# Kernel tuning notes

Measured on AMD Instinct MI355X. Metric: run time of the kernel, lower is better.

## Reference

```python
import jax, jax.numpy as jnp
import numpy as np


def setup_inputs() -> dict:
    key = jax.random.key(0)
    x = jax.random.normal(key, (8, 128, 64, 64), dtype=jnp.float32)
    return {"x": x}


def reference(x) -> jnp.ndarray:
    # x: [B, d, c, c]; original uses a raw view (row-major reshape), not a permute.
    B, d, c, _ = x.shape
    n = c * c
    fch = x.reshape(B, n, d)                      # [B, N, d] reinterpretation of memory
    # self-similarity attention (no scaling): softmax(fch @ fch^T)
    attn = jax.nn.softmax(jnp.einsum('bnd,bmd->bnm', fch, fch), axis=-1)  # [B, N, N]
    out = jnp.einsum('bnd,bnm->bdm', fch, attn)   # fch^T @ attn -> [B, d, N]
    return out.reshape(B, d, c, c)
```

## Files before the change

kernel.cpp:

```cpp
#include <hip/hip_runtime.h>


typedef __attribute__((ext_vector_type(8))) __bf16 bf16x8;
typedef __attribute__((ext_vector_type(4))) float f32x4;
typedef __attribute__((ext_vector_type(4))) unsigned int u32x4;

#define MFMA16(a, b, c) __builtin_amdgcn_mfma_f32_16x16x32_bf16((a), (b), (c), 0, 0, 0)
#define GLOAD16(g, l)                                                       \
  __builtin_amdgcn_global_load_lds(                                         \
      (const __attribute__((address_space(1))) void*)(g),                   \
      (__attribute__((address_space(3))) void*)(l), 16, 0, 0)
#define GLOAD4(g, l)                                                        \
  __builtin_amdgcn_global_load_lds(                                         \
      (const __attribute__((address_space(1))) void*)(g),                   \
      (__attribute__((address_space(3))) void*)(l), 4, 0, 0)

static constexpr int NT = 4096;
static constexpr int DD = 128;
static constexpr float L2E = 1.4426950408889634f;

__device__ __forceinline__ unsigned short bfc(float f) {
  return __builtin_bit_cast(unsigned short, (__bf16)f);
}
__device__ __forceinline__ float bf2f(unsigned short u) {
  return (float)__builtin_bit_cast(__bf16, u);
}

__global__ __launch_bounds__(256) void cab_prep(const float* __restrict__ x,
                                                ushort* __restrict__ Fbb,
                                                ushort* __restrict__ Ftb,
                                                float* __restrict__ nrm,
                                                float* __restrict__ bmax) {
  const int blk = blockIdx.x;
  const int b = blk & 7, n0 = (blk >> 3) * 64;
  const float* F = x + ((size_t)b * NT + n0) * DD;
  ushort* Fo = Fbb + ((size_t)b * NT + n0) * DD;
  ushort* To = Ftb + (size_t)b * DD * NT + n0;

  __shared__ ushort T[128 * 66];
  __shared__ float redw[4];

  const int t = threadIdx.x, seg = t & 15, rl = t >> 4;
  float lmax = 0.f;

#pragma unroll
  for (int i = 0; i < 4; ++i) {
    const int r = i * 16 + rl;
    float4 u = *(const float4*)(F + (size_t)r * DD + seg * 8);
    float4 v = *(const float4*)(F + (size_t)r * DD + seg * 8 + 4);
    ushort w[8] = {bfc(u.x), bfc(u.y), bfc(u.z), bfc(u.w),
                   bfc(v.x), bfc(v.y), bfc(v.z), bfc(v.w)};
    *(ushort4*)(Fo + (size_t)r * DD + seg * 8) = make_ushort4(w[0], w[1], w[2], w[3]);
    *(ushort4*)(Fo + (size_t)r * DD + seg * 8 + 4) = make_ushort4(w[4], w[5], w[6], w[7]);
    float s = 0.f;
#pragma unroll
    for (int j = 0; j < 8; ++j) {
      T[(seg * 8 + j) * 66 + r] = w[j];
      float f = bf2f(w[j]);
      s = fmaf(f, f, s);
    }
#pragma unroll
    for (int off = 1; off < 16; off <<= 1) s += __shfl_xor(s, off, 64);
    float rn = sqrtf(s);
    if (seg == 0) nrm[(size_t)b * NT + n0 + r] = rn;
    lmax = fmaxf(lmax, rn);
  }
#pragma unroll
  for (int off = 1; off < 64; off <<= 1) lmax = fmaxf(lmax, __shfl_xor(lmax, off, 64));
  if ((t & 63) == 0) redw[t >> 6] = lmax;
  __syncthreads();
  if (t == 0) bmax[blk] = fmaxf(fmaxf(redw[0], redw[1]), fmaxf(redw[2], redw[3]));

#pragma unroll
  for (int i = 0; i < 4; ++i) {
    int idx = i * 256 + t;
    int d = idx >> 3, ch = idx & 7;
    const ushort* p = &T[d * 66 + ch * 8];
    u32x4 q;
    q[0] = *(const unsigned*)(p + 0);
    q[1] = *(const unsigned*)(p + 2);
    q[2] = *(const unsigned*)(p + 4);
    q[3] = *(const unsigned*)(p + 6);
    *(u32x4*)(To + (size_t)d * NT + ch * 8) = q;
  }
}

__global__ __launch_bounds__(64) void cab_mx(const float* __restrict__ bmax,
                                             float* __restrict__ mxf) {
  const int b = blockIdx.x, l = threadIdx.x;
  float m = bmax[l * 8 + b];
#pragma unroll
  for (int off = 1; off < 64; off <<= 1) m = fmaxf(m, __shfl_xor(m, off, 64));
  if (l == 0) mxf[b] = m;
}

__global__ __launch_bounds__(256, 4) void cab_rowstats(const ushort* __restrict__ Fbb,
                                                       const float* __restrict__ nrm,
                                                       const float* __restrict__ mxf,
                                                       float* __restrict__ c2g) {
  const int b = blockIdx.x & 7;
  const int nb = (blockIdx.x >> 3) * 64;
  const ushort* Fb = Fbb + (size_t)b * NT * DD;

  const int t = threadIdx.x, lane = t & 63, wv = t >> 6;
  const int lcol = lane & 15, hi = lane >> 4;
  const int nh = wv >> 1, mq = wv & 1;

  __shared__ __align__(16) char FmB[2][16384];
  __shared__ float zred[64];

  int fmoff[4];
#pragma unroll
  for (int i = 0; i < 4; ++i) {
    int L = i * 256 + t;
    int m = L >> 4, c = (L & 15) ^ (m & 15);
    fmoff[i] = m * DD + c * 8;
  }

  bf16x8 afr[2][4];
#pragma unroll
  for (int nt = 0; nt < 2; ++nt)
#pragma unroll
    for (int ks = 0; ks < 4; ++ks)
      afr[nt][ks] = *(const bf16x8*)(Fb + (size_t)(nb + nh * 32 + nt * 16 + lcol) * DD +
                                     ks * 32 + hi * 8);

  const float mxv = mxf[b] * L2E;
  float nsh[8];
#pragma unroll
  for (int nt = 0; nt < 2; ++nt)
#pragma unroll
    for (int r = 0; r < 4; ++r)
      nsh[nt * 4 + r] = -nrm[(size_t)b * NT + nb + nh * 32 + nt * 16 + hi * 4 + r] * mxv;

#pragma unroll
  for (int i = 0; i < 4; ++i) GLOAD16(Fb + fmoff[i], &FmB[0][i * 4096 + wv * 1024]);
  __syncthreads();

  float zloc[8];
#pragma unroll
  for (int i = 0; i < 8; ++i) zloc[i] = 0.f;

  for (int s = 0; s < 64; ++s) {
    const int cur = s & 1;
    if (s < 63) {
      const ushort* src = Fb + (size_t)(s + 1) * 64 * DD;
#pragma unroll
      for (int i = 0; i < 4; ++i)
        GLOAD16(src + fmoff[i], &FmB[cur ^ 1][i * 4096 + wv * 1024]);
    }

    f32x4 sacc[2][2];
#pragma unroll
    for (int nt = 0; nt < 2; ++nt)
#pragma unroll
      for (int ms = 0; ms < 2; ++ms) sacc[nt][ms] = (f32x4){0.f, 0.f, 0.f, 0.f};
#pragma unroll
    for (int ms = 0; ms < 2; ++ms)
#pragma unroll
      for (int ks = 0; ks < 4; ++ks) {
        int ml = mq * 32 + ms * 16 + lcol;
        bf16x8 bb = *(const bf16x8*)&FmB[cur][ml * 256 + (((ks * 4 + hi) ^ lcol) << 4)];
#pragma unroll
        for (int nt = 0; nt < 2; ++nt) sacc[nt][ms] = MFMA16(afr[nt][ks], bb, sacc[nt][ms]);
      }
#pragma unroll
    for (int nt = 0; nt < 2; ++nt)
#pragma unroll
      for (int r = 0; r < 4; ++r)
        zloc[nt * 4 + r] += __builtin_amdgcn_exp2f(fmaf(sacc[nt][0][r], L2E, nsh[nt * 4 + r])) +
                            __builtin_amdgcn_exp2f(fmaf(sacc[nt][1][r], L2E, nsh[nt * 4 + r]));
    __syncthreads();
  }

#pragma unroll
  for (int i = 0; i < 8; ++i) {
#pragma unroll
    for (int off = 1; off < 16; off <<= 1) zloc[i] += __shfl_xor(zloc[i], off, 64);
  }
  if (mq == 1 && lcol == 0) {
#pragma unroll
    for (int i = 0; i < 8; ++i) zred[nh * 32 + (i >> 2) * 16 + hi * 4 + (i & 3)] = zloc[i];
  }
  __syncthreads();
  if (mq == 0 && lcol == 0) {
#pragma unroll
    for (int i = 0; i < 8; ++i) {
      int nloc = nh * 32 + (i >> 2) * 16 + hi * 4 + (i & 3);
      c2g[(size_t)b * NT + nb + nloc] = nsh[i] - __log2f(zloc[i] + zred[nloc]);
    }
  }
}

__global__ __launch_bounds__(256, 2) void cab_out(const ushort* __restrict__ Fbb,
                                                  const ushort* __restrict__ Ftb,
                                                  const float* __restrict__ c2g,
                                                  float* __restrict__ out) {
  const int b = blockIdx.x & 7, mb0 = (blockIdx.x >> 3) * 64;
  const ushort* Fb = Fbb + (size_t)b * NT * DD;
  const ushort* Ft = Ftb + (size_t)b * DD * NT;
  const float* c2p = c2g + (size_t)b * NT;

  const int t = threadIdx.x, lane = t & 63, wv = t >> 6;
  const int lcol = lane & 15, hi = lane >> 4;
  const int mh = wv & 1, nh = wv >> 1;

  __shared__ __align__(16) char LB[42496];
  char* FnB = LB;
  char* FttB = LB + 16384;
  char* Wt = LB + 32768;
  float* c2l = (float*)(LB + 41984);

  int fnoff[4], fttoff[4];
#pragma unroll
  for (int i = 0; i < 4; ++i) {
    int L = i * 256 + t;
    int n = L >> 4, cn = (L & 15) ^ (n & 15);
    fnoff[i] = n * DD + cn * 8;
    int d = L >> 3, cd = (L & 7) ^ (d & 7);
    fttoff[i] = d * NT + cd * 8;
  }

  bf16x8 fmf[2][4];
#pragma unroll
  for (int ms = 0; ms < 2; ++ms)
#pragma unroll
    for (int ks = 0; ks < 4; ++ks)
      fmf[ms][ks] = *(const bf16x8*)(Fb + (size_t)(mb0 + mh * 32 + ms * 16 + lcol) * DD +
                                     ks * 32 + hi * 8);

  f32x4 accO[8][2];
#pragma unroll
  for (int dt = 0; dt < 8; ++dt)
#pragma unroll
    for (int ms = 0; ms < 2; ++ms) accO[dt][ms] = (f32x4){0.f, 0.f, 0.f, 0.f};

#pragma unroll
  for (int i = 0; i < 4; ++i) GLOAD16(Fb + fnoff[i], &FnB[i * 4096 + wv * 1024]);
#pragma unroll
  for (int i = 0; i < 4; ++i) GLOAD16(Ft + fttoff[i], &FttB[i * 4096 + wv * 1024]);
  if (wv == 0) GLOAD4(c2p + lane, &c2l[0]);
  __syncthreads();

  const unsigned wtbase = wv * 2304;

  for (int s = 0; s < 64; ++s) {
    f32x4 sacc[2][2];
#pragma unroll
    for (int nt = 0; nt < 2; ++nt)
#pragma unroll
      for (int ms = 0; ms < 2; ++ms) sacc[nt][ms] = (f32x4){0.f, 0.f, 0.f, 0.f};
#pragma unroll
    for (int nt = 0; nt < 2; ++nt)
#pragma unroll
      for (int ks = 0; ks < 4; ++ks) {
        int n = (nh * 2 + nt) * 16 + lcol;
        bf16x8 a = *(const bf16x8*)&FnB[n * 256 + (((ks * 4 + hi) ^ lcol) << 4)];
#pragma unroll
        for (int ms = 0; ms < 2; ++ms) sacc[nt][ms] = MFMA16(a, fmf[ms][ks], sacc[nt][ms]);
      }
    bf16x8 a2[8];
#pragma unroll
    for (int dt = 0; dt < 8; ++dt)
      a2[dt] = *(const bf16x8*)&FttB[(dt * 16 + lcol) * 128 +
                                     (((nh * 4 + hi) ^ (lcol & 7)) << 4)];

    __syncthreads();

    if (s < 63) {
      const ushort* fs = Fb + (size_t)(s + 1) * 64 * DD;
      const ushort* ts = Ft + (s + 1) * 64;
#pragma unroll
      for (int i = 0; i < 4; ++i) GLOAD16(fs + fnoff[i], &FnB[i * 4096 + wv * 1024]);
#pragma unroll
      for (int i = 0; i < 4; ++i) GLOAD16(ts + fttoff[i], &FttB[i * 4096 + wv * 1024]);
      if (wv == 0) GLOAD4(c2p + (s + 1) * 64 + lane, &c2l[((s + 1) & 1) * 64]);
    }

#pragma unroll
    for (int nt = 0; nt < 2; ++nt) {
      float4 cv = *(const float4*)&c2l[(s & 1) * 64 + nh * 32 + nt * 16 + hi * 4];
#pragma unroll
      for (int ms = 0; ms < 2; ++ms) {
        ushort4 wp;
        wp.x = bfc(__builtin_amdgcn_exp2f(fmaf(sacc[nt][ms][0], L2E, cv.x)));
        wp.y = bfc(__builtin_amdgcn_exp2f(fmaf(sacc[nt][ms][1], L2E, cv.y)));
        wp.z = bfc(__builtin_amdgcn_exp2f(fmaf(sacc[nt][ms][2], L2E, cv.z)));
        wp.w = bfc(__builtin_amdgcn_exp2f(fmaf(sacc[nt][ms][3], L2E, cv.w)));
        *(ushort4*)&Wt[wtbase + (ms * 16 + lcol) * 72 + nt * 32 + hi * 8] = wp;
      }
    }
    bf16x8 b2[2];
#pragma unroll
    for (int ms = 0; ms < 2; ++ms) {
      const char* p = &Wt[wtbase + (ms * 16 + lcol) * 72 + hi * 16];
      uint2 lo = *(const uint2*)p;
      uint2 h2 = *(const uint2*)(p + 8);
      b2[ms] = __builtin_bit_cast(bf16x8, (u32x4){lo.x, lo.y, h2.x, h2.y});
    }
#pragma unroll
    for (int dt = 0; dt < 8; ++dt)
#pragma unroll
      for (int ms = 0; ms < 2; ++ms) accO[dt][ms] = MFMA16(a2[dt], b2[ms], accO[dt][ms]);

    __syncthreads();
  }

  float* red = (float*)LB;
  if (nh == 1) {
#pragma unroll
    for (int dt = 0; dt < 8; ++dt)
#pragma unroll
      for (int ms = 0; ms < 2; ++ms)
#pragma unroll
        for (int r = 0; r < 4; ++r)
          red[mh * 4096 + (dt * 8 + ms * 4 + r) * 64 + lane] = accO[dt][ms][r];
  }
  __syncthreads();
  if (nh == 0) {
    float* Ob = out + (size_t)b * DD * NT;
#pragma unroll
    for (int dt = 0; dt < 8; ++dt)
#pragma unroll
      for (int ms = 0; ms < 2; ++ms)
#pragma unroll
        for (int r = 0; r < 4; ++r) {
          float v = accO[dt][ms][r] + red[mh * 4096 + (dt * 8 + ms * 4 + r) * 64 + lane];
          Ob[(size_t)(dt * 16 + hi * 4 + r) * NT + mb0 + mh * 32 + ms * 16 + lcol] = v;
        }
  }
}

extern "C" void kernel_launch(void* const* d_in, const int* in_sizes, int n_in,
                              void* d_out, int out_size, void* d_ws, size_t ws_size,
                              hipStream_t stream) {
  const float* x = (const float*)d_in[0];
  float* out = (float*)d_out;
  char* ws = (char*)d_ws;
  ushort* Fbb = (ushort*)ws;
  ushort* Ftb = (ushort*)(ws + (8u << 20));
  float* nrm = (float*)(ws + (16u << 20));
  float* bmax = (float*)(ws + (16u << 20) + 131072);
  float* mxf = (float*)(ws + (16u << 20) + 133120);
  float* c2 = (float*)(ws + (16u << 20) + 134144);

  hipLaunchKernelGGL(cab_prep, dim3(512), dim3(256), 0, stream, x, Fbb, Ftb, nrm, bmax);
  hipLaunchKernelGGL(cab_mx, dim3(8), dim3(64), 0, stream, bmax, mxf);
  hipLaunchKernelGGL(cab_rowstats, dim3(512), dim3(256), 0, stream, Fbb, nrm, mxf, c2);
  hipLaunchKernelGGL(cab_out, dim3(512), dim3(256), 0, stream, Fbb, Ftb, c2, out);
}
```

Measured before the change: 139.7 us.

## Split key dimension in half across blocks for rowstats and output kernels

Doubles the grid of both the row-statistics and output kernels by splitting the 4096-long key loop into two halves. Partial softmax denominators are written to a scratch buffer and combined by a new small kernel that computes the log-normaliser. Output partials are accumulated with float atomicAdd into a zeroed output. This targets low occupancy: 512 blocks on a 256-CU part, with cab_out limited to two blocks per CU. The cost is an extra memset, an extra launch, and atomic traffic on the output.

```diff
diff --git a/kernel.cpp b/kernel.cpp
--- a/kernel.cpp
+++ b/kernel.cpp
@@ -97,9 +97,10 @@
 __global__ __launch_bounds__(256, 4) void cab_rowstats(const ushort* __restrict__ Fbb,
                                                        const float* __restrict__ nrm,
                                                        const float* __restrict__ mxf,
-                                                       float* __restrict__ c2g) {
+                                                       float* __restrict__ zpart) {
   const int b = blockIdx.x & 7;
-  const int nb = (blockIdx.x >> 3) * 64;
+  const int nb = ((blockIdx.x >> 3) & 63) * 64;
+  const int mhalf = blockIdx.x >> 9;
   const ushort* Fb = Fbb + (size_t)b * NT * DD;
 
   const int t = threadIdx.x, lane = t & 63, wv = t >> 6;
@@ -133,18 +134,19 @@
     for (int r = 0; r < 4; ++r)
       nsh[nt * 4 + r] = -nrm[(size_t)b * NT + nb + nh * 32 + nt * 16 + hi * 4 + r] * mxv;
 
-#pragma unroll
-  for (int i = 0; i < 4; ++i) GLOAD16(Fb + fmoff[i], &FmB[0][i * 4096 + wv * 1024]);
+  const ushort* Fm0 = Fb + (size_t)mhalf * 2048 * DD;
+#pragma unroll
+  for (int i = 0; i < 4; ++i) GLOAD16(Fm0 + fmoff[i], &FmB[0][i * 4096 + wv * 1024]);
   __syncthreads();
 
   float zloc[8];
 #pragma unroll
   for (int i = 0; i < 8; ++i) zloc[i] = 0.f;
 
-  for (int s = 0; s < 64; ++s) {
+  for (int s = 0; s < 32; ++s) {
     const int cur = s & 1;
-    if (s < 63) {
-      const ushort* src = Fb + (size_t)(s + 1) * 64 * DD;
+    if (s < 31) {
+      const ushort* src = Fm0 + (size_t)(s + 1) * 64 * DD;
 #pragma unroll
       for (int i = 0; i < 4; ++i)
         GLOAD16(src + fmoff[i], &FmB[cur ^ 1][i * 4096 + wv * 1024]);
@@ -187,16 +189,28 @@
 #pragma unroll
     for (int i = 0; i < 8; ++i) {
       int nloc = nh * 32 + (i >> 2) * 16 + hi * 4 + (i & 3);
-      c2g[(size_t)b * NT + nb + nloc] = nsh[i] - __log2f(zloc[i] + zred[nloc]);
-    }
-  }
+      zpart[(size_t)mhalf * 8 * NT + (size_t)b * NT + nb + nloc] = zloc[i] + zred[nloc];
+    }
+  }
+}
+
+__global__ __launch_bounds__(256) void cab_c2(const float* __restrict__ zpart,
+                                              const float* __restrict__ nrm,
+                                              const float* __restrict__ mxf,
+                                              float* __restrict__ c2g) {
+  int i = blockIdx.x * 256 + threadIdx.x;
+  int b = i >> 12;
+  float z = zpart[i] + zpart[8 * NT + i];
+  float nsh = -nrm[i] * (mxf[b] * L2E);
+  c2g[i] = nsh - __log2f(z);
 }
 
 __global__ __launch_bounds__(256, 2) void cab_out(const ushort* __restrict__ Fbb,
                                                   const ushort* __restrict__ Ftb,
                                                   const float* __restrict__ c2g,
                                                   float* __restrict__ out) {
-  const int b = blockIdx.x & 7, mb0 = (blockIdx.x >> 3) * 64;
+  const int b = blockIdx.x & 7, mb0 = ((blockIdx.x >> 3) & 63) * 64;
+  const int s0 = (blockIdx.x >> 9) * 32, s1 = s0 + 32;
   const ushort* Fb = Fbb + (size_t)b * NT * DD;
   const ushort* Ft = Ftb + (size_t)b * DD * NT;
   const float* c2p = c2g + (size_t)b * NT;
@@ -236,15 +250,17 @@
     for (int ms = 0; ms < 2; ++ms) accO[dt][ms] = (f32x4){0.f, 0.f, 0.f, 0.f};
 
 #pragma unroll
-  for (int i = 0; i < 4; ++i) GLOAD16(Fb + fnoff[i], &FnB[i * 4096 + wv * 1024]);
-#pragma unroll
-  for (int i = 0; i < 4; ++i) GLOAD16(Ft + fttoff[i], &FttB[i * 4096 + wv * 1024]);
-  if (wv == 0) GLOAD4(c2p + lane, &c2l[0]);
+  for (int i = 0; i < 4; ++i)
+    GLOAD16(Fb + (size_t)s0 * 64 * DD + fnoff[i], &FnB[i * 4096 + wv * 1024]);
+#pragma unroll
+  for (int i = 0; i < 4; ++i)
+    GLOAD16(Ft + s0 * 64 + fttoff[i], &FttB[i * 4096 + wv * 1024]);
+  if (wv == 0) GLOAD4(c2p + s0 * 64 + lane, &c2l[(s0 & 1) * 64]);
   __syncthreads();
 
   const unsigned wtbase = wv * 2304;
 
-  for (int s = 0; s < 64; ++s) {
+  for (int s = s0; s < s1; ++s) {
     f32x4 sacc[2][2];
 #pragma unroll
     for (int nt = 0; nt < 2; ++nt)
@@ -267,7 +283,7 @@
 
     __syncthreads();
 
-    if (s < 63) {
+    if (s < s1 - 1) {
       const ushort* fs = Fb + (size_t)(s + 1) * 64 * DD;
       const ushort* ts = Ft + (s + 1) * 64;
 #pragma unroll
@@ -326,7 +342,7 @@
 #pragma unroll
         for (int r = 0; r < 4; ++r) {
           float v = accO[dt][ms][r] + red[mh * 4096 + (dt * 8 + ms * 4 + r) * 64 + lane];
-          Ob[(size_t)(dt * 16 + hi * 4 + r) * NT + mb0 + mh * 32 + ms * 16 + lcol] = v;
+          atomicAdd(&Ob[(size_t)(dt * 16 + hi * 4 + r) * NT + mb0 + mh * 32 + ms * 16 + lcol], v);
         }
   }
 }
@@ -343,9 +359,13 @@
   float* bmax = (float*)(ws + (16u << 20) + 131072);
   float* mxf = (float*)(ws + (16u << 20) + 133120);
   float* c2 = (float*)(ws + (16u << 20) + 134144);
+  float* zpart = (float*)(ws + (16u << 20) + 265216);
+
+  hipMemsetAsync(out, 0, (size_t)out_size * sizeof(float), stream);
 
   hipLaunchKernelGGL(cab_prep, dim3(512), dim3(256), 0, stream, x, Fbb, Ftb, nrm, bmax);
   hipLaunchKernelGGL(cab_mx, dim3(8), dim3(64), 0, stream, bmax, mxf);
-  hipLaunchKernelGGL(cab_rowstats, dim3(512), dim3(256), 0, stream, Fbb, nrm, mxf, c2);
-  hipLaunchKernelGGL(cab_out, dim3(512), dim3(256), 0, stream, Fbb, Ftb, c2, out);
-}
+  hipLaunchKernelGGL(cab_rowstats, dim3(1024), dim3(256), 0, stream, Fbb, nrm, mxf, zpart);
+  hipLaunchKernelGGL(cab_c2, dim3(128), dim3(256), 0, stream, zpart, nrm, mxf, c2);
+  hipLaunchKernelGGL(cab_out, dim3(1024), dim3(256), 0, stream, Fbb, Ftb, c2, out);
+}
```

Result: slower. 171.1 us (+22.4%).

## Pre-swizzle transposed features into MFMA fragment layout and double-buffer Fn tile

Applied to the files above, without the earlier changes.

The prep kernel now writes the transposed bf16 features in a layout that matches the MFMA A-fragment order of the output kernel. The output kernel can then load each lane's a2 operands straight from global memory into registers, with no staging through LDS. The freed LDS holds a second Fn buffer, so the next tile is prefetched into the other buffer at the start of each iteration and the middle __syncthreads is dropped. The trade-off is more per-iteration global/L2 traffic going directly to registers, whose latency must be hidden by the score MFMAs and the softmax step.

```diff
diff --git a/kernel.cpp b/kernel.cpp
--- a/kernel.cpp
+++ b/kernel.cpp
@@ -28,16 +28,16 @@
 
 __global__ __launch_bounds__(256) void cab_prep(const float* __restrict__ x,
                                                 ushort* __restrict__ Fbb,
-                                                ushort* __restrict__ Ftb,
+                                                ushort* __restrict__ FtF,
                                                 float* __restrict__ nrm,
                                                 float* __restrict__ bmax) {
   const int blk = blockIdx.x;
   const int b = blk & 7, n0 = (blk >> 3) * 64;
   const float* F = x + ((size_t)b * NT + n0) * DD;
   ushort* Fo = Fbb + ((size_t)b * NT + n0) * DD;
-  ushort* To = Ftb + (size_t)b * DD * NT + n0;
-
-  __shared__ ushort T[128 * 66];
+  ushort* To = FtF + (size_t)b * DD * NT;
+
+  __shared__ ushort T[128 * 68];
   __shared__ float redw[4];
 
   const int t = threadIdx.x, seg = t & 15, rl = t >> 4;
@@ -55,7 +55,7 @@
     float s = 0.f;
 #pragma unroll
     for (int j = 0; j < 8; ++j) {
-      T[(seg * 8 + j) * 66 + r] = w[j];
+      T[(seg * 8 + j) * 68 + r] = w[j];
       float f = bf2f(w[j]);
       s = fmaf(f, f, s);
     }
@@ -74,14 +74,13 @@
 #pragma unroll
   for (int i = 0; i < 4; ++i) {
     int idx = i * 256 + t;
-    int d = idx >> 3, ch = idx & 7;
-    const ushort* p = &T[d * 66 + ch * 8];
-    u32x4 q;
-    q[0] = *(const unsigned*)(p + 0);
-    q[1] = *(const unsigned*)(p + 2);
-    q[2] = *(const unsigned*)(p + 4);
-    q[3] = *(const unsigned*)(p + 6);
-    *(u32x4*)(To + (size_t)d * NT + ch * 8) = q;
+    int nh = idx >> 9, dt = (idx >> 6) & 7, ln = idx & 63;
+    int d = dt * 16 + (ln & 15), nl = nh * 32 + (ln >> 4) * 8;
+    const ushort* p = &T[d * 68 + nl];
+    uint2 q0 = *(const uint2*)p;
+    uint2 q1 = *(const uint2*)(p + 4);
+    u32x4 q = {q0.x, q0.y, q1.x, q1.y};
+    *(u32x4*)(To + (size_t)(((n0 >> 6) * 2 + nh) * 8 + dt) * 512 + ln * 8) = q;
   }
 }
 
@@ -193,12 +192,12 @@
 }
 
 __global__ __launch_bounds__(256, 2) void cab_out(const ushort* __restrict__ Fbb,
-                                                  const ushort* __restrict__ Ftb,
+                                                  const ushort* __restrict__ FtF,
                                                   const float* __restrict__ c2g,
                                                   float* __restrict__ out) {
   const int b = blockIdx.x & 7, mb0 = (blockIdx.x >> 3) * 64;
   const ushort* Fb = Fbb + (size_t)b * NT * DD;
-  const ushort* Ft = Ftb + (size_t)b * DD * NT;
+  const ushort* Fr = FtF + (size_t)b * DD * NT;
   const float* c2p = c2g + (size_t)b * NT;
 
   const int t = threadIdx.x, lane = t & 63, wv = t >> 6;
@@ -207,18 +206,15 @@
 
   __shared__ __align__(16) char LB[42496];
   char* FnB = LB;
-  char* FttB = LB + 16384;
   char* Wt = LB + 32768;
   float* c2l = (float*)(LB + 41984);
 
-  int fnoff[4], fttoff[4];
+  int fnoff[4];
 #pragma unroll
   for (int i = 0; i < 4; ++i) {
     int L = i * 256 + t;
     int n = L >> 4, cn = (L & 15) ^ (n & 15);
     fnoff[i] = n * DD + cn * 8;
-    int d = L >> 3, cd = (L & 7) ^ (d & 7);
-    fttoff[i] = d * NT + cd * 8;
   }
 
   bf16x8 fmf[2][4];
@@ -237,14 +233,28 @@
 
 #pragma unroll
   for (int i = 0; i < 4; ++i) GLOAD16(Fb + fnoff[i], &FnB[i * 4096 + wv * 1024]);
-#pragma unroll
-  for (int i = 0; i < 4; ++i) GLOAD16(Ft + fttoff[i], &FttB[i * 4096 + wv * 1024]);
   if (wv == 0) GLOAD4(c2p + lane, &c2l[0]);
   __syncthreads();
 
   const unsigned wtbase = wv * 2304;
+  const ushort* a2w = Fr + (size_t)(nh * 8) * 512 + lane * 8;
 
   for (int s = 0; s < 64; ++s) {
+    const int cur = s & 1;
+
+    const ushort* ap = a2w + (size_t)s * 8192;
+    bf16x8 a2[8];
+#pragma unroll
+    for (int dt = 0; dt < 8; ++dt) a2[dt] = *(const bf16x8*)(ap + dt * 512);
+
+    if (s < 63) {
+      const ushort* fs = Fb + (size_t)(s + 1) * 64 * DD;
+#pragma unroll
+      for (int i = 0; i < 4; ++i)
+        GLOAD16(fs + fnoff[i], &FnB[(cur ^ 1) * 16384 + i * 4096 + wv * 1024]);
+      if (wv == 0) GLOAD4(c2p + (s + 1) * 64 + lane, &c2l[((s + 1) & 1) * 64]);
+    }
+
     f32x4 sacc[2][2];
 #pragma unroll
     for (int nt = 0; nt < 2; ++nt)
@@ -255,27 +265,11 @@
 #pragma unroll
       for (int ks = 0; ks < 4; ++ks) {
         int n = (nh * 2 + nt) * 16 + lcol;
-        bf16x8 a = *(const bf16x8*)&FnB[n * 256 + (((ks * 4 + hi) ^ lcol) << 4)];
+        bf16x8 a = *(const bf16x8*)&FnB[cur * 16384 + n * 256 +
+                                        (((ks * 4 + hi) ^ lcol) << 4)];
 #pragma unroll
         for (int ms = 0; ms < 2; ++ms) sacc[nt][ms] = MFMA16(a, fmf[ms][ks], sacc[nt][ms]);
       }
-    bf16x8 a2[8];
-#pragma unroll
-    for (int dt = 0; dt < 8; ++dt)
-      a2[dt] = *(const bf16x8*)&FttB[(dt * 16 + lcol) * 128 +
-                                     (((nh * 4 + hi) ^ (lcol & 7)) << 4)];
-
-    __syncthreads();
-
-    if (s < 63) {
-      const ushort* fs = Fb + (size_t)(s + 1) * 64 * DD;
-      const ushort* ts = Ft + (s + 1) * 64;
-#pragma unroll
-      for (int i = 0; i < 4; ++i) GLOAD16(fs + fnoff[i], &FnB[i * 4096 + wv * 1024]);
-#pragma unroll
-      for (int i = 0; i < 4; ++i) GLOAD16(ts + fttoff[i], &FttB[i * 4096 + wv * 1024]);
-      if (wv == 0) GLOAD4(c2p + (s + 1) * 64 + lane, &c2l[((s + 1) & 1) * 64]);
-    }
 
 #pragma unroll
     for (int nt = 0; nt < 2; ++nt) {
@@ -290,6 +284,7 @@
         *(ushort4*)&Wt[wtbase + (ms * 16 + lcol) * 72 + nt * 32 + hi * 8] = wp;
       }
     }
+
     bf16x8 b2[2];
 #pragma unroll
     for (int ms = 0; ms < 2; ++ms) {
@@ -338,14 +333,14 @@
   float* out = (float*)d_out;
   char* ws = (char*)d_ws;
   ushort* Fbb = (ushort*)ws;
-  ushort* Ftb = (ushort*)(ws + (8u << 20));
+  ushort* FtF = (ushort*)(ws + (8u << 20));
   float* nrm = (float*)(ws + (16u << 20));
   float* bmax = (float*)(ws + (16u << 20) + 131072);
   float* mxf = (float*)(ws + (16u << 20) + 133120);
   float* c2 = (float*)(ws + (16u << 20) + 134144);
 
-  hipLaunchKernelGGL(cab_prep, dim3(512), dim3(256), 0, stream, x, Fbb, Ftb, nrm, bmax);
+  hipLaunchKernelGGL(cab_prep, dim3(512), dim3(256), 0, stream, x, Fbb, FtF, nrm, bmax);
   hipLaunchKernelGGL(cab_mx, dim3(8), dim3(64), 0, stream, bmax, mxf);
   hipLaunchKernelGGL(cab_rowstats, dim3(512), dim3(256), 0, stream, Fbb, nrm, mxf, c2);
-  hipLaunchKernelGGL(cab_out, dim3(512), dim3(256), 0, stream, Fbb, Ftb, c2, out);
-}
+  hipLaunchKernelGGL(cab_out, dim3(512), dim3(256), 0, stream, Fbb, FtF, c2, out);
+}
```

Measured after the change: 132.0 us, median of 2. 5.5% less time.
